# Performance work log

Hardware: AMD Instinct MI355X
Metric: run time of the kernel (lower is better)

Reference implementation:

```python
import jax, jax.numpy as jnp
import numpy as np

B, D, H = 4096, 1024, 1024


def setup_inputs() -> dict:
    key = jax.random.key(0)
    ks = jax.random.split(key, 20)
    s_in = 1.0 / np.sqrt(D)
    s_hid = 1.0 / np.sqrt(H)
    inp = {
        "x_t": jax.random.normal(ks[0], (B, D), dtype=jnp.float32),
        "h_t_1": jax.random.normal(ks[1], (B, H), dtype=jnp.float32),
        "c_t_1": jax.random.normal(ks[2], (B, H), dtype=jnp.float32),
        # input-to-hidden weights (nn.Linear: y = x @ W.T + b), stacked i,f,o,z
        "W": jax.random.uniform(ks[3], (4, H, D), minval=-s_in, maxval=s_in, dtype=jnp.float32),
        "bW": jax.random.uniform(ks[4], (4, H), minval=-s_in, maxval=s_in, dtype=jnp.float32),
        # hidden-to-hidden weights, stacked i,f,o,z
        "U": jax.random.uniform(ks[5], (4, H, H), minval=-s_hid, maxval=s_hid, dtype=jnp.float32),
        "bU": jax.random.uniform(ks[6], (4, H), minval=-s_hid, maxval=s_hid, dtype=jnp.float32),
    }
    return inp


def reference(x_t, h_t_1, c_t_1, W, bW, U, bU):
    # Two stacked GEMMs: [B,D]x[4,H,D] -> [4,B,H], [B,H]x[4,H,H] -> [4,B,H]
    gx = jnp.einsum("bd,ghd->gbh", x_t, W) + bW[:, None, :]
    gh = jnp.einsum("bh,gkh->gbk", h_t_1, U) + bU[:, None, :]
    g = gx + gh  # [4, B, H] pre-activations for i, f, o, z
    i = jax.nn.sigmoid(g[0])
    f = jax.nn.sigmoid(g[1])
    o = jax.nn.sigmoid(g[2])
    z = jnp.tanh(g[3])
    c_t = i * z + f * c_t_1
    h_t = o * jnp.tanh(c_t)
    return (h_t, c_t)
```

## Files before the change

### kernel.cpp

```cpp
#include <hip/hip_runtime.h>
#include <math.h>

#define Mm 4096
#define Nn 4096
#define Kk 2048

typedef __bf16 bf16x8 __attribute__((ext_vector_type(8)));
typedef float f32x4 __attribute__((ext_vector_type(4)));

__device__ __forceinline__ unsigned short f2bf(float f) {
    union { float f; unsigned u; } v; v.f = f;
    unsigned r = v.u + 0x7FFFu + ((v.u >> 16) & 1u);
    return (unsigned short)(r >> 16);
}

__device__ __forceinline__ float fast_tanh(float x) {
    return 1.f - 2.f / (1.f + __expf(2.f * x));
}

__global__ void pack_bf16(const float* __restrict__ x, const float* __restrict__ h,
                          const float* __restrict__ W, const float* __restrict__ U,
                          const float* __restrict__ bW, const float* __restrict__ bU,
                          unsigned short* __restrict__ Xc, unsigned short* __restrict__ Wc,
                          float* __restrict__ bsum) {
    if (blockIdx.x == 0) {
#pragma unroll
        for (int j = 0; j < 16; ++j) {
            int n = threadIdx.x * 16 + j;
            int hh = n >> 2, g = n & 3;
            bsum[n] = bW[g * 1024 + hh] + bU[g * 1024 + hh];
        }
    }
    const int PER = (4096 * 1024) / 4;
    for (int t = blockIdx.x * blockDim.x + threadIdx.x; t < 4 * PER;
         t += gridDim.x * blockDim.x) {
        int region = t >> 20;
        int i = t & (PER - 1);
        int row = i >> 8;
        int c4  = i & 255;
        const float* src = (region == 0) ? x : (region == 1) ? h : (region == 2) ? W : U;
        float4 v = reinterpret_cast<const float4*>(src)[i];
        ushort4 o;
        o.x = f2bf(v.x); o.y = f2bf(v.y); o.z = f2bf(v.z); o.w = f2bf(v.w);
        if (region < 2) {
            *reinterpret_cast<ushort4*>(Xc + (size_t)row * 2048 + (region << 10) + c4 * 4) = o;
        } else {
            int g = row >> 10, hh = row & 1023;
            *reinterpret_cast<ushort4*>(Wc + (size_t)(hh * 4 + g) * 2048 + ((region & 1) << 10) + c4 * 4) = o;
        }
    }
}

__device__ __forceinline__ void gl16(const void* g, void* l) {
    __builtin_amdgcn_global_load_lds(
        (const __attribute__((address_space(1))) void*)g,
        (__attribute__((address_space(3))) void*)l, 16, 0, 0);
}

#define A_OFF(p, ah) (((p) * 2 + (ah)) * 16384)
#define B_OFF(p, hb) (65536 + ((p) * 2 + (hb)) * 16384)

__global__ __launch_bounds__(512, 2) void gemm_8ph(const unsigned short* __restrict__ A,
                                                   const unsigned short* __restrict__ Bw,
                                                   const float* __restrict__ bsum,
                                                   const float* __restrict__ cprev,
                                                   float* __restrict__ out) {
    extern __shared__ char lds[];
    const int tid = threadIdx.x, lane = tid & 63, wave = tid >> 6;
    const int wm = wave >> 2, wn = wave & 3;

    const int bid = blockIdx.x;
    const int swz = (bid & 7) * 32 + (bid >> 3);
    const int bm = swz & 15, bn = swz >> 4;
    const size_t Crow0 = (size_t)bm * 256, Ccol0 = (size_t)bn * 256;

    const int srow = wave * 8 + (lane >> 3);
    const int scolswz = (((lane & 7) ^ (lane >> 3)) << 4);
    const char* aS[2][2];
    const char* bS[2][2];
#pragma unroll
    for (int ah = 0; ah < 2; ++ah)
#pragma unroll
        for (int j = 0; j < 2; ++j) {
            aS[ah][j] = (const char*)A  + (size_t)(Crow0 + ah * 128 + j * 64 + srow) * 4096 + scolswz;
            bS[ah][j] = (const char*)Bw + (size_t)(Ccol0 + ah * 128 + j * 64 + srow) * 4096 + scolswz;
        }

#define STG_A(p, ah, kb) do { \
        gl16(aS[ah][0] + (kb), lds + A_OFF(p, ah) + wave * 1024); \
        gl16(aS[ah][1] + (kb), lds + A_OFF(p, ah) + 8192 + wave * 1024); } while (0)
#define STG_B(p, hb, kb) do { \
        gl16(bS[hb][0] + (kb), lds + B_OFF(p, hb) + wave * 1024); \
        gl16(bS[hb][1] + (kb), lds + B_OFF(p, hb) + 8192 + wave * 1024); } while (0)

    const int arowB = (wm * 64 + (lane & 15)) * 128;
    const int browB = ((wn & 1) * 64 + (lane & 15)) * 128;
    const int c0 = (((lane >> 4) << 4)) ^ ((lane & 7) << 4);
    const int c1 = (64 + ((lane >> 4) << 4)) ^ ((lane & 7) << 4);
    const int bhb = wn >> 1;

#define LDA(p, ah, mfl, ck) (*(const bf16x8*)(lds + A_OFF(p, ah) + arowB + (mfl) * 2048 + (ck)))
#define LDB(p, nf, ck)      (*(const bf16x8*)(lds + B_OFF(p, bhb) + browB + (nf) * 2048 + (ck)))

    f32x4 acc[2][4][4] = {};

#define MF8(ah, mf, ak0, ak1) \
    acc[ah][mf][0] = __builtin_amdgcn_mfma_f32_16x16x32_bf16(ak0, b00, acc[ah][mf][0], 0, 0, 0); \
    acc[ah][mf][0] = __builtin_amdgcn_mfma_f32_16x16x32_bf16(ak1, b01, acc[ah][mf][0], 0, 0, 0); \
    acc[ah][mf][1] = __builtin_amdgcn_mfma_f32_16x16x32_bf16(ak0, b10, acc[ah][mf][1], 0, 0, 0); \
    acc[ah][mf][1] = __builtin_amdgcn_mfma_f32_16x16x32_bf16(ak1, b11, acc[ah][mf][1], 0, 0, 0); \
    acc[ah][mf][2] = __builtin_amdgcn_mfma_f32_16x16x32_bf16(ak0, b20, acc[ah][mf][2], 0, 0, 0); \
    acc[ah][mf][2] = __builtin_amdgcn_mfma_f32_16x16x32_bf16(ak1, b21, acc[ah][mf][2], 0, 0, 0); \
    acc[ah][mf][3] = __builtin_amdgcn_mfma_f32_16x16x32_bf16(ak0, b30, acc[ah][mf][3], 0, 0, 0); \
    acc[ah][mf][3] = __builtin_amdgcn_mfma_f32_16x16x32_bf16(ak1, b31, acc[ah][mf][3], 0, 0, 0);

#define PH_TAIL \
    __builtin_amdgcn_s_barrier(); \
    asm volatile("s_waitcnt lgkmcnt(0)" ::: "memory"); \
    __builtin_amdgcn_s_setprio(1);

#define PH_END \
    __builtin_amdgcn_s_setprio(0); \
    __builtin_amdgcn_s_barrier();

#define GROUP(p, kbA1, kbT2) \
    { \
        bf16x8 b00 = LDB(p, 0, c0), b01 = LDB(p, 0, c1), b10 = LDB(p, 1, c0), b11 = LDB(p, 1, c1); \
        bf16x8 b20 = LDB(p, 2, c0), b21 = LDB(p, 2, c1), b30 = LDB(p, 3, c0), b31 = LDB(p, 3, c1); \
        {  \
            bf16x8 a00 = LDA(p, 0, 0, c0), a01 = LDA(p, 0, 0, c1); \
            bf16x8 a10 = LDA(p, 0, 1, c0), a11 = LDA(p, 0, 1, c1); \
            STG_A((p) ^ 1, 1, kbA1); \
            PH_TAIL MF8(0, 0, a00, a01) MF8(0, 1, a10, a11) PH_END \
        } \
        {  \
            bf16x8 a00 = LDA(p, 0, 2, c0), a01 = LDA(p, 0, 2, c1); \
            bf16x8 a10 = LDA(p, 0, 3, c0), a11 = LDA(p, 0, 3, c1); \
            STG_B(p, 0, kbT2); \
            PH_TAIL MF8(0, 2, a00, a01) MF8(0, 3, a10, a11) PH_END \
        } \
        {  \
            bf16x8 a00 = LDA(p, 1, 0, c0), a01 = LDA(p, 1, 0, c1); \
            bf16x8 a10 = LDA(p, 1, 1, c0), a11 = LDA(p, 1, 1, c1); \
            STG_A(p, 0, kbT2); \
            PH_TAIL MF8(1, 0, a00, a01) MF8(1, 1, a10, a11) PH_END \
        } \
        {  \
            bf16x8 a00 = LDA(p, 1, 2, c0), a01 = LDA(p, 1, 2, c1); \
            bf16x8 a10 = LDA(p, 1, 3, c0), a11 = LDA(p, 1, 3, c1); \
            STG_B(p, 1, kbT2); \
            __builtin_amdgcn_s_barrier(); \
            asm volatile("s_waitcnt lgkmcnt(0)" ::: "memory"); \
            __builtin_amdgcn_s_setprio(1); \
            MF8(1, 2, a00, a01) MF8(1, 3, a10, a11) \
            __builtin_amdgcn_s_setprio(0); \
            asm volatile("s_waitcnt vmcnt(6)" ::: "memory"); \
            __builtin_amdgcn_s_barrier(); \
        } \
    }

    STG_B(0, 0, 0);
    STG_A(0, 0, 0);
    STG_B(0, 1, 0);
    STG_A(0, 1, 0);
    STG_B(1, 0, 128);
    STG_A(1, 0, 128);
    STG_B(1, 1, 128);
    asm volatile("s_waitcnt vmcnt(6)" ::: "memory");
    __builtin_amdgcn_s_barrier();

    for (int it = 0; it < 16; ++it) {
        const int t0 = 2 * it;
        const size_t kA1_0 = (size_t)(t0 + 1) * 128;
        const size_t kT2_0 = (t0 + 2 <= 31) ? (size_t)(t0 + 2) * 128 : 0;
        const size_t kA1_1 = kT2_0;
        const size_t kT2_1 = (t0 + 3 <= 31) ? (size_t)(t0 + 3) * 128 : 0;
        GROUP(0, kA1_0, kT2_0)
        GROUP(1, kA1_1, kT2_1)
    }

    const int Hbase = (int)(Ccol0 >> 2);

    float cp[2][16];
#pragma unroll
    for (int ah = 0; ah < 2; ++ah)
#pragma unroll
        for (int i = 0; i < 16; ++i)
            cp[ah][i] = cprev[(Crow0 + ah * 128 + i * 8 + wave) * 1024 + Hbase + lane];
    const f32x4 bs = *(const f32x4*)(bsum + (size_t)(Hbase + lane) * 4);

    __syncthreads();

#pragma unroll
    for (int ah = 0; ah < 2; ++ah) {
        if (ah) __syncthreads();
        const int er0 = (lane >> 4) * 4;
        const int ecc = lane & 15;
#pragma unroll
        for (int mf = 0; mf < 4; ++mf)
#pragma unroll
            for (int r = 0; r < 4; ++r) {
                const int lrow = wm * 64 + mf * 16 + er0 + r;
                const int sw = (lrow & 4) << 4;
#pragma unroll
                for (int nf = 0; nf < 4; ++nf) {
                    const int col = wn * 64 + nf * 16 + ecc;
                    *(float*)(lds + lrow * 1024 + ((col * 4) ^ sw)) = acc[ah][mf][nf][r];
                }
            }
        __syncthreads();
#pragma unroll
        for (int i = 0; i < 16; ++i) {
            const int lrow = i * 8 + wave;
            const int sw = (lrow & 4) << 4;
            f32x4 g4 = *(const f32x4*)(lds + lrow * 1024 + ((lane * 16) ^ sw));
            const size_t bg = Crow0 + ah * 128 + lrow;
            const size_t oidx = bg * 1024 + Hbase + lane;
            float gi = g4[0] + bs[0], gf = g4[1] + bs[1];
            float go = g4[2] + bs[2], gz = g4[3] + bs[3];
            float iv = 1.f / (1.f + __expf(-gi));
            float fv = 1.f / (1.f + __expf(-gf));
            float ov = 1.f / (1.f + __expf(-go));
            float zv = fast_tanh(gz);
            float cc = fmaf(iv, zv, fv * cp[ah][i]);
            float hv = ov * fast_tanh(cc);
            out[oidx] = hv;
            out[(1 << 22) + oidx] = cc;
        }
    }
}

extern "C" void kernel_launch(void* const* d_in, const int* in_sizes, int n_in,
                              void* d_out, int out_size, void* d_ws, size_t ws_size,
                              hipStream_t stream) {
    const float* x  = (const float*)d_in[0];
    const float* h  = (const float*)d_in[1];
    const float* c  = (const float*)d_in[2];
    const float* W  = (const float*)d_in[3];
    const float* bW = (const float*)d_in[4];
    const float* U  = (const float*)d_in[5];
    const float* bU = (const float*)d_in[6];
    float* out = (float*)d_out;

    char* ws = (char*)d_ws;
    unsigned short* Xc = (unsigned short*)ws;
    unsigned short* Wc = (unsigned short*)(ws + ((size_t)16 << 20));
    float* bsum = (float*)(ws + ((size_t)32 << 20));

    (void)hipFuncSetAttribute((const void*)gemm_8ph,
                              hipFuncAttributeMaxDynamicSharedMemorySize, 131072);

    hipLaunchKernelGGL(pack_bf16, dim3(2048), dim3(256), 0, stream,
                       x, h, W, U, bW, bU, Xc, Wc, bsum);
    hipLaunchKernelGGL(gemm_8ph, dim3(256), dim3(512), 131072, stream,
                       Xc, Wc, bsum, c, out);
}
```

Measured before the change: 87.46 us.

## Software-pipeline LDS fragment reads ahead of MFMA phases in GROUP

Restructures the per-tile inner schedule so that the A fragments for the next MFMA phase are loaded from LDS while the current phase's MFMAs run, using two register sets. It also cuts the barrier count per phase and drops the explicit lgkmcnt(0) waits, leaving the compiler to insert the waits. The aim is to hide LDS read latency behind matrix work and reduce synchronization stalls. The cost is more registers live at once, and the relaxed barrier placement may change how global-to-LDS stores line up with reads.

```diff
diff --git a/kernel.cpp b/kernel.cpp
--- a/kernel.cpp
+++ b/kernel.cpp
@@ -114,49 +114,40 @@
     acc[ah][mf][3] = __builtin_amdgcn_mfma_f32_16x16x32_bf16(ak0, b30, acc[ah][mf][3], 0, 0, 0); \
     acc[ah][mf][3] = __builtin_amdgcn_mfma_f32_16x16x32_bf16(ak1, b31, acc[ah][mf][3], 0, 0, 0);
 
-#define PH_TAIL \
-    __builtin_amdgcn_s_barrier(); \
-    asm volatile("s_waitcnt lgkmcnt(0)" ::: "memory"); \
-    __builtin_amdgcn_s_setprio(1);
-
-#define PH_END \
-    __builtin_amdgcn_s_setprio(0); \
-    __builtin_amdgcn_s_barrier();
-
 #define GROUP(p, kbA1, kbT2) \
     { \
         bf16x8 b00 = LDB(p, 0, c0), b01 = LDB(p, 0, c1), b10 = LDB(p, 1, c0), b11 = LDB(p, 1, c1); \
         bf16x8 b20 = LDB(p, 2, c0), b21 = LDB(p, 2, c1), b30 = LDB(p, 3, c0), b31 = LDB(p, 3, c1); \
-        {  \
-            bf16x8 a00 = LDA(p, 0, 0, c0), a01 = LDA(p, 0, 0, c1); \
-            bf16x8 a10 = LDA(p, 0, 1, c0), a11 = LDA(p, 0, 1, c1); \
-            STG_A((p) ^ 1, 1, kbA1); \
-            PH_TAIL MF8(0, 0, a00, a01) MF8(0, 1, a10, a11) PH_END \
-        } \
-        {  \
-            bf16x8 a00 = LDA(p, 0, 2, c0), a01 = LDA(p, 0, 2, c1); \
-            bf16x8 a10 = LDA(p, 0, 3, c0), a11 = LDA(p, 0, 3, c1); \
-            STG_B(p, 0, kbT2); \
-            PH_TAIL MF8(0, 2, a00, a01) MF8(0, 3, a10, a11) PH_END \
-        } \
-        {  \
-            bf16x8 a00 = LDA(p, 1, 0, c0), a01 = LDA(p, 1, 0, c1); \
-            bf16x8 a10 = LDA(p, 1, 1, c0), a11 = LDA(p, 1, 1, c1); \
-            STG_A(p, 0, kbT2); \
-            PH_TAIL MF8(1, 0, a00, a01) MF8(1, 1, a10, a11) PH_END \
-        } \
-        {  \
-            bf16x8 a00 = LDA(p, 1, 2, c0), a01 = LDA(p, 1, 2, c1); \
-            bf16x8 a10 = LDA(p, 1, 3, c0), a11 = LDA(p, 1, 3, c1); \
-            STG_B(p, 1, kbT2); \
-            __builtin_amdgcn_s_barrier(); \
-            asm volatile("s_waitcnt lgkmcnt(0)" ::: "memory"); \
-            __builtin_amdgcn_s_setprio(1); \
-            MF8(1, 2, a00, a01) MF8(1, 3, a10, a11) \
-            __builtin_amdgcn_s_setprio(0); \
-            asm volatile("s_waitcnt vmcnt(6)" ::: "memory"); \
-            __builtin_amdgcn_s_barrier(); \
-        } \
+        bf16x8 a00 = LDA(p, 0, 0, c0), a01 = LDA(p, 0, 0, c1); \
+        bf16x8 a10 = LDA(p, 0, 1, c0), a11 = LDA(p, 0, 1, c1); \
+        STG_A((p) ^ 1, 1, kbA1); \
+        __builtin_amdgcn_s_barrier(); \
+        bf16x8 n00 = LDA(p, 0, 2, c0), n01 = LDA(p, 0, 2, c1); \
+        bf16x8 n10 = LDA(p, 0, 3, c0), n11 = LDA(p, 0, 3, c1); \
+        __builtin_amdgcn_s_setprio(1); \
+        MF8(0, 0, a00, a01) MF8(0, 1, a10, a11) \
+        __builtin_amdgcn_s_setprio(0); \
+        __builtin_amdgcn_s_barrier(); \
+        STG_B(p, 0, kbT2); \
+        a00 = LDA(p, 1, 0, c0); a01 = LDA(p, 1, 0, c1); \
+        a10 = LDA(p, 1, 1, c0); a11 = LDA(p, 1, 1, c1); \
+        __builtin_amdgcn_s_setprio(1); \
+        MF8(0, 2, n00, n01) MF8(0, 3, n10, n11) \
+        __builtin_amdgcn_s_setprio(0); \
+        __builtin_amdgcn_s_barrier(); \
+        STG_A(p, 0, kbT2); \
+        n00 = LDA(p, 1, 2, c0); n01 = LDA(p, 1, 2, c1); \
+        n10 = LDA(p, 1, 3, c0); n11 = LDA(p, 1, 3, c1); \
+        __builtin_amdgcn_s_setprio(1); \
+        MF8(1, 0, a00, a01) MF8(1, 1, a10, a11) \
+        __builtin_amdgcn_s_setprio(0); \
+        __builtin_amdgcn_s_barrier(); \
+        STG_B(p, 1, kbT2); \
+        __builtin_amdgcn_s_setprio(1); \
+        MF8(1, 2, n00, n01) MF8(1, 3, n10, n11) \
+        __builtin_amdgcn_s_setprio(0); \
+        asm volatile("s_waitcnt vmcnt(6)" ::: "memory"); \
+        __builtin_amdgcn_s_barrier(); \
     }
 
     STG_B(0, 0, 0);
```

After: 86.93 us. Within noise of the previous version (-0.6%).

## Permute gate weight layout so epilogue reads gates from registers, drop LDS staging

Applied to the files above, without the earlier changes.

Reorders the packed weight rows so that each 16-column MFMA fragment holds a single gate, which puts the four gates of one hidden unit in the same lane across the four accumulator fragments. The epilogue then computes the LSTM cell directly from registers, removing the LDS write/read round trip and its barriers. The MFMA issue order is also interleaved so consecutive instructions write different accumulators, shortening dependent chains. In exchange, global stores and cprev loads now cover 16 consecutive floats per row instead of 64, so they coalesce less well.

```diff
diff --git a/kernel.cpp b/kernel.cpp
--- a/kernel.cpp
+++ b/kernel.cpp
@@ -46,7 +46,8 @@
             *reinterpret_cast<ushort4*>(Xc + (size_t)row * 2048 + (region << 10) + c4 * 4) = o;
         } else {
             int g = row >> 10, hh = row & 1023;
-            *reinterpret_cast<ushort4*>(Wc + (size_t)(hh * 4 + g) * 2048 + ((region & 1) << 10) + c4 * 4) = o;
+            int np = ((hh >> 4) << 6) + (g << 4) + (hh & 15);
+            *reinterpret_cast<ushort4*>(Wc + (size_t)np * 2048 + ((region & 1) << 10) + c4 * 4) = o;
         }
     }
 }
@@ -104,15 +105,24 @@
 
     f32x4 acc[2][4][4] = {};
 
-#define MF8(ah, mf, ak0, ak1) \
-    acc[ah][mf][0] = __builtin_amdgcn_mfma_f32_16x16x32_bf16(ak0, b00, acc[ah][mf][0], 0, 0, 0); \
-    acc[ah][mf][0] = __builtin_amdgcn_mfma_f32_16x16x32_bf16(ak1, b01, acc[ah][mf][0], 0, 0, 0); \
-    acc[ah][mf][1] = __builtin_amdgcn_mfma_f32_16x16x32_bf16(ak0, b10, acc[ah][mf][1], 0, 0, 0); \
-    acc[ah][mf][1] = __builtin_amdgcn_mfma_f32_16x16x32_bf16(ak1, b11, acc[ah][mf][1], 0, 0, 0); \
-    acc[ah][mf][2] = __builtin_amdgcn_mfma_f32_16x16x32_bf16(ak0, b20, acc[ah][mf][2], 0, 0, 0); \
-    acc[ah][mf][2] = __builtin_amdgcn_mfma_f32_16x16x32_bf16(ak1, b21, acc[ah][mf][2], 0, 0, 0); \
-    acc[ah][mf][3] = __builtin_amdgcn_mfma_f32_16x16x32_bf16(ak0, b30, acc[ah][mf][3], 0, 0, 0); \
-    acc[ah][mf][3] = __builtin_amdgcn_mfma_f32_16x16x32_bf16(ak1, b31, acc[ah][mf][3], 0, 0, 0);
+#define MFMA(a, b, c) __builtin_amdgcn_mfma_f32_16x16x32_bf16(a, b, c, 0, 0, 0)
+#define MF16(ah, mfA, mfB, p00, p01, p10, p11) \
+    acc[ah][mfA][0] = MFMA(p00, b00, acc[ah][mfA][0]); \
+    acc[ah][mfA][1] = MFMA(p00, b10, acc[ah][mfA][1]); \
+    acc[ah][mfA][2] = MFMA(p00, b20, acc[ah][mfA][2]); \
+    acc[ah][mfA][3] = MFMA(p00, b30, acc[ah][mfA][3]); \
+    acc[ah][mfB][0] = MFMA(p10, b00, acc[ah][mfB][0]); \
+    acc[ah][mfB][1] = MFMA(p10, b10, acc[ah][mfB][1]); \
+    acc[ah][mfB][2] = MFMA(p10, b20, acc[ah][mfB][2]); \
+    acc[ah][mfB][3] = MFMA(p10, b30, acc[ah][mfB][3]); \
+    acc[ah][mfA][0] = MFMA(p01, b01, acc[ah][mfA][0]); \
+    acc[ah][mfA][1] = MFMA(p01, b11, acc[ah][mfA][1]); \
+    acc[ah][mfA][2] = MFMA(p01, b21, acc[ah][mfA][2]); \
+    acc[ah][mfA][3] = MFMA(p01, b31, acc[ah][mfA][3]); \
+    acc[ah][mfB][0] = MFMA(p11, b01, acc[ah][mfB][0]); \
+    acc[ah][mfB][1] = MFMA(p11, b11, acc[ah][mfB][1]); \
+    acc[ah][mfB][2] = MFMA(p11, b21, acc[ah][mfB][2]); \
+    acc[ah][mfB][3] = MFMA(p11, b31, acc[ah][mfB][3]);
 
 #define PH_TAIL \
     __builtin_amdgcn_s_barrier(); \
@@ -131,19 +141,19 @@
             bf16x8 a00 = LDA(p, 0, 0, c0), a01 = LDA(p, 0, 0, c1); \
             bf16x8 a10 = LDA(p, 0, 1, c0), a11 = LDA(p, 0, 1, c1); \
             STG_A((p) ^ 1, 1, kbA1); \
-            PH_TAIL MF8(0, 0, a00, a01) MF8(0, 1, a10, a11) PH_END \
+            PH_TAIL MF16(0, 0, 1, a00, a01, a10, a11) PH_END \
         } \
         {  \
             bf16x8 a00 = LDA(p, 0, 2, c0), a01 = LDA(p, 0, 2, c1); \
             bf16x8 a10 = LDA(p, 0, 3, c0), a11 = LDA(p, 0, 3, c1); \
             STG_B(p, 0, kbT2); \
-            PH_TAIL MF8(0, 2, a00, a01) MF8(0, 3, a10, a11) PH_END \
+            PH_TAIL MF16(0, 2, 3, a00, a01, a10, a11) PH_END \
         } \
         {  \
             bf16x8 a00 = LDA(p, 1, 0, c0), a01 = LDA(p, 1, 0, c1); \
             bf16x8 a10 = LDA(p, 1, 1, c0), a11 = LDA(p, 1, 1, c1); \
             STG_A(p, 0, kbT2); \
-            PH_TAIL MF8(1, 0, a00, a01) MF8(1, 1, a10, a11) PH_END \
+            PH_TAIL MF16(1, 0, 1, a00, a01, a10, a11) PH_END \
         } \
         {  \
             bf16x8 a00 = LDA(p, 1, 2, c0), a01 = LDA(p, 1, 2, c1); \
@@ -152,7 +162,7 @@
             __builtin_amdgcn_s_barrier(); \
             asm volatile("s_waitcnt lgkmcnt(0)" ::: "memory"); \
             __builtin_amdgcn_s_setprio(1); \
-            MF8(1, 2, a00, a01) MF8(1, 3, a10, a11) \
+            MF16(1, 2, 3, a00, a01, a10, a11) \
             __builtin_amdgcn_s_setprio(0); \
             asm volatile("s_waitcnt vmcnt(6)" ::: "memory"); \
             __builtin_amdgcn_s_barrier(); \
@@ -179,55 +189,43 @@
         GROUP(1, kA1_1, kT2_1)
     }
 
-    const int Hbase = (int)(Ccol0 >> 2);
-
-    float cp[2][16];
+    const int hl = lane & 15;
+    const int er0 = (lane >> 4) * 4;
+    const int myh = (int)(Ccol0 >> 2) + wn * 16 + hl;
+    const f32x4 bs = *(const f32x4*)(bsum + (size_t)myh * 4);
+
+    float cp[2][4][4];
 #pragma unroll
     for (int ah = 0; ah < 2; ++ah)
 #pragma unroll
-        for (int i = 0; i < 16; ++i)
-            cp[ah][i] = cprev[(Crow0 + ah * 128 + i * 8 + wave) * 1024 + Hbase + lane];
-    const f32x4 bs = *(const f32x4*)(bsum + (size_t)(Hbase + lane) * 4);
-
-    __syncthreads();
-
-#pragma unroll
-    for (int ah = 0; ah < 2; ++ah) {
-        if (ah) __syncthreads();
-        const int er0 = (lane >> 4) * 4;
-        const int ecc = lane & 15;
-#pragma unroll
         for (int mf = 0; mf < 4; ++mf)
 #pragma unroll
+            for (int r = 0; r < 4; ++r)
+                cp[ah][mf][r] = cprev[(size_t)(Crow0 + ah * 128 + wm * 64 + mf * 16 + er0 + r) * 1024 + myh];
+
+#pragma unroll
+    for (int ah = 0; ah < 2; ++ah)
+#pragma unroll
+        for (int mf = 0; mf < 4; ++mf)
+#pragma unroll
             for (int r = 0; r < 4; ++r) {
-                const int lrow = wm * 64 + mf * 16 + er0 + r;
-                const int sw = (lrow & 4) << 4;
-#pragma unroll
-                for (int nf = 0; nf < 4; ++nf) {
-                    const int col = wn * 64 + nf * 16 + ecc;
-                    *(float*)(lds + lrow * 1024 + ((col * 4) ^ sw)) = acc[ah][mf][nf][r];
-                }
+                float gi = acc[ah][mf][0][r] + bs[0];
+                float gf = acc[ah][mf][1][r] + bs[1];
+                float go = acc[ah][mf][2][r] + bs[2];
+                float gz = acc[ah][mf][3][r] + bs[3];
+                float iv = 1.f / (1.f + __expf(-gi));
+                float fv = 1.f / (1.f + __expf(-gf));
+                float ov = 1.f / (1.f + __expf(-go));
+                float zv = fast_tanh(gz);
+                float cc = fmaf(iv, zv, fv * cp[ah][mf][r]);
+                float hv = ov * fast_tanh(cc);
+                const size_t oidx =
+                    (size_t)(Crow0 + ah * 128 + wm * 64 + mf * 16 + er0 + r) * 1024 + myh;
+                out[oidx] = hv;
+                out[(1 << 22) + oidx] = cc;
             }
-        __syncthreads();
-#pragma unroll
-        for (int i = 0; i < 16; ++i) {
-            const int lrow = i * 8 + wave;
-            const int sw = (lrow & 4) << 4;
-            f32x4 g4 = *(const f32x4*)(lds + lrow * 1024 + ((lane * 16) ^ sw));
-            const size_t bg = Crow0 + ah * 128 + lrow;
-            const size_t oidx = bg * 1024 + Hbase + lane;
-            float gi = g4[0] + bs[0], gf = g4[1] + bs[1];
-            float go = g4[2] + bs[2], gz = g4[3] + bs[3];
-            float iv = 1.f / (1.f + __expf(-gi));
-            float fv = 1.f / (1.f + __expf(-gf));
-            float ov = 1.f / (1.f + __expf(-go));
-            float zv = fast_tanh(gz);
-            float cc = fmaf(iv, zv, fv * cp[ah][i]);
-            float hv = ov * fast_tanh(cc);
-            out[oidx] = hv;
-            out[(1 << 22) + oidx] = cc;
-        }
-    }
+
+    asm volatile("s_waitcnt vmcnt(0)" ::: "memory");
 }
 
 extern "C" void kernel_launch(void* const* d_in, const int* in_sizes, int n_in,
```

After: 84.83 us. 1.03x faster.
